# Performance work log

Hardware: AMD Instinct MI355X
Metric: run time of the kernel (lower is better)

Reference implementation:

```python
import jax, jax.numpy as jnp
import numpy as np

N = 100000   # n_nodes
D = 64       # feature dim
E = 1000000  # n_edges (avg degree 10)
L = 10       # filter_count_L
ALPHA = 0.3
EPS = 1e-8


def setup_inputs() -> dict:
    key = jax.random.key(0)
    k1, k2, k3, k4 = jax.random.split(key, 4)
    edge_src = jax.random.randint(k1, (E,), 0, N)
    edge_dst = jax.random.randint(k2, (E,), 0, N)
    # positive edge weights, scaled roughly like a degree-normalized adjacency
    edge_vals = jax.random.uniform(k3, (E,), dtype=jnp.float32) * 0.2
    X = jax.random.normal(k4, (N, D), dtype=jnp.float32)
    # hyperbolic GPR weights: alpha * (1-alpha)^(1.5*l)  (reset_parameters)
    l_idx = jnp.arange(L + 1, dtype=jnp.float32)
    manifold_weights = ALPHA * (1.0 - ALPHA) ** (l_idx * 1.5)
    return {
        "X": X,
        "edge_vals": edge_vals,
        "manifold_weights": manifold_weights,
        "edge_src": edge_src,
        "edge_dst": edge_dst,
    }


def reference(X, edge_vals, manifold_weights, edge_src, edge_dst):
    n = X.shape[0]

    def spmm(H):
        # A_tilde_n @ H with A given as COO edge list:
        # out[dst] += val * H[src]
        return jax.ops.segment_sum(edge_vals[:, None] * H[edge_src], edge_dst,
                                   num_segments=n)

    H = X
    Z = manifold_weights[0] * H  # l = 0 term
    for l in range(1, L + 1):
        H = spmm(H)
        # hyperbolic renorm: H <- H / (||H|| + eps) * tanh(||H|| + eps)
        Hn = jnp.linalg.norm(H, axis=1, keepdims=True)
        H = H / (Hn + EPS) * jnp.tanh(Hn + EPS)
        Z = Z + manifold_weights[l] * H
    return Z
```

## Files before the change

kernel.cpp:

```cpp
#include <hip/hip_runtime.h>
#include <hip/hip_fp16.h>

#define DFEAT 64
#define EPSV 1e-8f
#define CHUNK 4096
#define CAP   6144

typedef unsigned int uint;
typedef unsigned char uchar;

__device__ __forceinline__ uint h2_as_uint(__half2 h) {
    union { __half2 h; uint u; } c; c.h = h; return c.u;
}
__device__ __forceinline__ __half2 uint_as_h2(uint u) {
    union { uint u; __half2 h; } c; c.u = u; return c.h;
}
__device__ __forceinline__ uint hpack2(float lo, float hi) {
    __half2 h;
    h.x = __float2half_rn(lo);
    h.y = __float2half_rn(hi);
    return h2_as_uint(h);
}

__global__ __launch_bounds__(256) void prep_kernel(const float* __restrict__ X,
                                                   const float* __restrict__ mw,
                                                   float* __restrict__ Z,
                                                   uint* __restrict__ Xh, int nq) {
    int i = blockIdx.x * blockDim.x + threadIdx.x;
    if (i >= nq) return;
    float w0 = mw[0];
    float4 x = ((const float4*)X)[i];
    ((float4*)Z)[i] = make_float4(w0 * x.x, w0 * x.y, w0 * x.z, w0 * x.w);
    ((uint2*)Xh)[i] = make_uint2(hpack2(x.x, x.y), hpack2(x.z, x.w));
}

__global__ __launch_bounds__(256) void partial_sum_kernel(const int* __restrict__ in,
                                                          int* __restrict__ part, int n) {
    __shared__ int s[256];
    int t = threadIdx.x;
    int i = blockIdx.x * 256 + t;
    s[t] = (i < n) ? in[i] : 0;
    __syncthreads();
    for (int off = 128; off; off >>= 1) {
        if (t < off) s[t] += s[t + off];
        __syncthreads();
    }
    if (t == 0) part[blockIdx.x] = s[0];
}

__global__ __launch_bounds__(1024) void scan_partials_kernel(int* __restrict__ part, int nb) {
    __shared__ int s[1024];
    int t = threadIdx.x;
    s[t] = (t < nb) ? part[t] : 0;
    __syncthreads();
    for (int off = 1; off < 1024; off <<= 1) {
        int x = (t >= off) ? s[t - off] : 0;
        __syncthreads();
        s[t] += x;
        __syncthreads();
    }
    if (t < nb) part[t] = (t == 0) ? 0 : s[t - 1];
    if (t == 0) part[nb] = s[1023];
}

__global__ __launch_bounds__(256) void scan_final_kernel(const int* __restrict__ in,
                                                         const int* __restrict__ part,
                                                         int* __restrict__ out,
                                                         int n, int nb) {
    __shared__ int s[256];
    int b = blockIdx.x, t = threadIdx.x;
    int i = b * 256 + t;
    s[t] = (i < n) ? in[i] : 0;
    __syncthreads();
    for (int off = 1; off < 256; off <<= 1) {
        int x = (t >= off) ? s[t - off] : 0;
        __syncthreads();
        s[t] += x;
        __syncthreads();
    }
    if (i < n) out[i] = part[b] + ((t == 0) ? 0 : s[t - 1]);
    if (i == 0) out[n] = part[nb];
}

__global__ __launch_bounds__(256) void bucket_hist_kernel(const int* __restrict__ dst,
                                                          int* __restrict__ counts,
                                                          int e, int nbuck, int nblk) {
    __shared__ int h[512];
    int t = threadIdx.x, blk = blockIdx.x;
    for (int i = t; i < 512; i += 256) h[i] = 0;
    __syncthreads();
    int base = blk * CHUNK;
    #pragma unroll
    for (int k = 0; k < CHUNK / 256; ++k) {
        int i = base + k * 256 + t;
        if (i < e) atomicAdd(&h[dst[i] >> 8], 1);
    }
    __syncthreads();
    for (int b = t; b < nbuck; b += 256) counts[b * nblk + blk] = h[b];
}

__global__ __launch_bounds__(256) void bucket_scatter_kernel(
        const int* __restrict__ src, const int* __restrict__ dst,
        const float* __restrict__ val, const int* __restrict__ cbase,
        uint* __restrict__ rec, uchar* __restrict__ lrow,
        int e, int nbuck, int nblk) {
    __shared__ int cur[512];
    int t = threadIdx.x, blk = blockIdx.x;
    for (int b = t; b < nbuck; b += 256) cur[b] = cbase[b * nblk + blk];
    __syncthreads();
    int base = blk * CHUNK;
    #pragma unroll
    for (int k = 0; k < CHUNK / 256; ++k) {
        int i = base + k * 256 + t;
        if (i < e) {
            int d = dst[i];
            int b = d >> 8;
            int p = atomicAdd(&cur[b], 1);
            uint vb = (uint)__half_as_ushort(__float2half_rn(val[i])) & 0x7fffu;
            rec[p]  = (uint)src[i] | (vb << 17);
            lrow[p] = (uchar)(d & 255);
        }
    }
}

__global__ __launch_bounds__(256) void bucket_sort_kernel(
        const uint* __restrict__ rec, const uchar* __restrict__ lrow,
        const int* __restrict__ cbase, int* __restrict__ deg,
        uint* __restrict__ csr, int n, int e, int nbuck, int nblk) {
    __shared__ uint  lr[CAP];
    __shared__ uchar ll[CAP];
    __shared__ uint  so[CAP];
    __shared__ int   sc[256];
    __shared__ int   cur[256];
    int b = blockIdx.x, t = threadIdx.x;
    int s0 = cbase[b * nblk];
    int s1 = (b == nbuck - 1) ? e : cbase[(b + 1) * nblk];
    int cnt = s1 - s0;
    if (cnt > CAP) cnt = CAP;
    for (int i = t; i < cnt; i += 256) { lr[i] = rec[s0 + i]; ll[i] = lrow[s0 + i]; }
    sc[t] = 0;
    __syncthreads();
    for (int i = t; i < cnt; i += 256) atomicAdd(&sc[ll[i]], 1);
    __syncthreads();
    int row = b * 256 + t;
    int myDeg = sc[t];
    if (row < n) deg[row] = myDeg;
    for (int off = 1; off < 256; off <<= 1) {
        int x = (t >= off) ? sc[t - off] : 0;
        __syncthreads();
        sc[t] += x;
        __syncthreads();
    }
    cur[t] = sc[t] - myDeg;
    __syncthreads();
    for (int i = t; i < cnt; i += 256) {
        int p = atomicAdd(&cur[ll[i]], 1);
        so[p] = lr[i];
    }
    __syncthreads();
    for (int i = t; i < cnt; i += 256) csr[s0 + i] = so[i];
}

__global__ __launch_bounds__(256) void spmm_renorm_kernel(
        const uint* __restrict__ Hin, uint* __restrict__ Hout,
        float* __restrict__ Z, const int* __restrict__ row_ptr,
        const uint* __restrict__ csr, const float* __restrict__ mw, int l, int n) {
    int wave = (blockIdx.x * blockDim.x + threadIdx.x) >> 6;
    int lane = threadIdx.x & 63;
    int rs = lane >> 5;
    int g  = (lane >> 3) & 3;
    int lg = lane & 7;
    int row = wave * 2 + rs;
    if (wave * 2 >= n) return;
    bool valid = (row < n);
    int beg = 0, end = 0;
    if (valid) { beg = row_ptr[row]; end = row_ptr[row + 1]; }
    const uint4* H4 = (const uint4*)Hin;
    __half2 hz = uint_as_h2(0u);
    __half2 hacc[4] = {hz, hz, hz, hz};
    int j = beg + g;
    for (; j + 4 < end; j += 8) {
        uint ua = csr[j];
        uint ub = csr[j + 4];
        uint4 qa = H4[(ua & 0x1ffffu) * 8u + (uint)lg];
        uint4 qb = H4[(ub & 0x1ffffu) * 8u + (uint)lg];
        uint va = ua >> 17;
        uint vb = ub >> 17;
        __half2 va2 = uint_as_h2(va | (va << 16));
        __half2 vb2 = uint_as_h2(vb | (vb << 16));
        hacc[0] = __hfma2(va2, uint_as_h2(qa.x), hacc[0]);
        hacc[1] = __hfma2(va2, uint_as_h2(qa.y), hacc[1]);
        hacc[2] = __hfma2(va2, uint_as_h2(qa.z), hacc[2]);
        hacc[3] = __hfma2(va2, uint_as_h2(qa.w), hacc[3]);
        hacc[0] = __hfma2(vb2, uint_as_h2(qb.x), hacc[0]);
        hacc[1] = __hfma2(vb2, uint_as_h2(qb.y), hacc[1]);
        hacc[2] = __hfma2(vb2, uint_as_h2(qb.z), hacc[2]);
        hacc[3] = __hfma2(vb2, uint_as_h2(qb.w), hacc[3]);
    }
    if (j < end) {
        uint u  = csr[j];
        uint4 q = H4[(u & 0x1ffffu) * 8u + (uint)lg];
        uint v = u >> 17;
        __half2 v2 = uint_as_h2(v | (v << 16));
        hacc[0] = __hfma2(v2, uint_as_h2(q.x), hacc[0]);
        hacc[1] = __hfma2(v2, uint_as_h2(q.y), hacc[1]);
        hacc[2] = __hfma2(v2, uint_as_h2(q.z), hacc[2]);
        hacc[3] = __hfma2(v2, uint_as_h2(q.w), hacc[3]);
    }
    #pragma unroll
    for (int off = 8; off <= 16; off <<= 1) {
        #pragma unroll
        for (int k = 0; k < 4; ++k) {
            uint o = __shfl_xor(h2_as_uint(hacc[k]), off);
            hacc[k] = __hadd2(hacc[k], uint_as_h2(o));
        }
    }
    float acc[8];
    #pragma unroll
    for (int k = 0; k < 4; ++k) {
        float2 f = __half22float2(hacc[k]);
        acc[2 * k]     = f.x;
        acc[2 * k + 1] = f.y;
    }
    float sq = 0.f;
    #pragma unroll
    for (int k = 0; k < 8; ++k) sq += acc[k] * acc[k];
    #pragma unroll
    for (int off = 1; off <= 4; off <<= 1) sq += __shfl_xor(sq, off);
    float nrm = sqrtf(sq) + EPSV;
    float ex = __expf(2.0f * nrm);
    float th = 1.0f - 2.0f * __builtin_amdgcn_rcpf(ex + 1.0f);
    float scale = th * __builtin_amdgcn_rcpf(nrm);
    if (valid) {
        if (g == 0) {
            __half sh = __float2half_rn(scale);
            __half2 s2; s2.x = sh; s2.y = sh;
            uint4 o;
            o.x = h2_as_uint(__hmul2(hacc[0], s2));
            o.y = h2_as_uint(__hmul2(hacc[1], s2));
            o.z = h2_as_uint(__hmul2(hacc[2], s2));
            o.w = h2_as_uint(__hmul2(hacc[3], s2));
            ((uint4*)Hout)[(uint)row * 8u + (uint)lg] = o;
        } else if (g == 1) {
            float ws = mw[l] * scale;
            float4* Z4 = (float4*)Z;
            uint zi = (uint)row * 16u + (uint)lg * 2u;
            float4 z0 = Z4[zi];
            z0.x += ws * acc[0]; z0.y += ws * acc[1];
            z0.z += ws * acc[2]; z0.w += ws * acc[3];
            Z4[zi] = z0;
        } else if (g == 2) {
            float ws = mw[l] * scale;
            float4* Z4 = (float4*)Z;
            uint zi = (uint)row * 16u + (uint)lg * 2u + 1u;
            float4 z1 = Z4[zi];
            z1.x += ws * acc[4]; z1.y += ws * acc[5];
            z1.z += ws * acc[6]; z1.w += ws * acc[7];
            Z4[zi] = z1;
        }
    }
}

extern "C" void kernel_launch(void* const* d_in, const int* in_sizes, int n_in,
                              void* d_out, int out_size, void* d_ws, size_t ws_size,
                              hipStream_t stream) {
    const float* X         = (const float*)d_in[0];
    const float* edge_vals = (const float*)d_in[1];
    const float* mw        = (const float*)d_in[2];
    const int*   edge_src  = (const int*)d_in[3];
    const int*   edge_dst  = (const int*)d_in[4];

    int nd = in_sizes[0];
    int n  = nd / DFEAT;
    int e  = in_sizes[1];
    int L  = in_sizes[2] - 1;
    float* Z = (float*)d_out;

    int nbuck = (n + 255) >> 8;
    int nblk  = (e + CHUNK - 1) / CHUNK;
    int n1    = nbuck * nblk;

    char* ws = (char*)d_ws;
    size_t off = 0;
    auto alloc = [&](size_t bytes) -> void* {
        void* p = ws + off;
        off = (off + bytes + 255) & ~(size_t)255;
        return p;
    };
    uint*  Xh      = (uint*) alloc((size_t)nd * 2);
    uint*  Ha      = (uint*) alloc((size_t)nd * 2);
    uint*  Hb      = (uint*) alloc((size_t)nd * 2);
    uint*  csr     = (uint*) alloc((size_t)e * 4);
    uint*  rec     = (uint*) alloc((size_t)e * 4);
    uchar* lrowb   = (uchar*)alloc((size_t)e);
    int*   counts  = (int*)  alloc((size_t)(n1 + 1) * 4);
    int*   cbase   = (int*)  alloc((size_t)(n1 + 1) * 4);
    int*   deg     = (int*)  alloc((size_t)n * 4);
    int*   row_ptr = (int*)  alloc((size_t)(n + 1) * 4);
    int*   part    = (int*)  alloc((size_t)1025 * 4);

    bucket_hist_kernel<<<nblk, 256, 0, stream>>>(edge_dst, counts, e, nbuck, nblk);
    int nb1 = (n1 + 255) / 256;
    partial_sum_kernel<<<nb1, 256, 0, stream>>>(counts, part, n1);
    scan_partials_kernel<<<1, 1024, 0, stream>>>(part, nb1);
    scan_final_kernel<<<nb1, 256, 0, stream>>>(counts, part, cbase, n1, nb1);
    bucket_scatter_kernel<<<nblk, 256, 0, stream>>>(edge_src, edge_dst, edge_vals,
                                                    cbase, rec, lrowb, e, nbuck, nblk);
    bucket_sort_kernel<<<nbuck, 256, 0, stream>>>(rec, lrowb, cbase, deg, csr,
                                                  n, e, nbuck, nblk);
    int nb2 = (n + 255) / 256;
    partial_sum_kernel<<<nb2, 256, 0, stream>>>(deg, part, n);
    scan_partials_kernel<<<1, 1024, 0, stream>>>(part, nb2);
    scan_final_kernel<<<nb2, 256, 0, stream>>>(deg, part, row_ptr, n, nb2);

    int nq = nd / 4;
    prep_kernel<<<(nq + 255) / 256, 256, 0, stream>>>(X, mw, Z, Xh, nq);

    int spmm_blocks = (n + 7) / 8;
    const uint* Hin = Xh;
    uint* Hout = Ha;
    for (int l = 1; l <= L; ++l) {
        spmm_renorm_kernel<<<spmm_blocks, 256, 0, stream>>>(
            Hin, Hout, Z, row_ptr, csr, mw, l, n);
        Hin  = Hout;
        Hout = (Hout == Ha) ? Hb : Ha;
    }
}
```

Before: 444.9 us.

## Defer Z accumulation to a final combine pass over stored fp16 layers

Each propagation step now writes its renormalised fp16 H into its own slice of a new buffer instead of overwriting a ping-pong pair. The SpMM kernel no longer does an fp32 read-modify-write of Z every iteration. A single combine kernel at the end reads X and all L stored layers and writes Z once. This removes repeated full-size fp32 Z traffic per layer, at the cost of L times more workspace and a Z sum built from fp16-rounded H instead of fp32 accumulators.

```diff
diff --git a/kernel.cpp b/kernel.cpp
--- a/kernel.cpp
+++ b/kernel.cpp
@@ -23,15 +23,32 @@
 }
 
 __global__ __launch_bounds__(256) void prep_kernel(const float* __restrict__ X,
-                                                   const float* __restrict__ mw,
-                                                   float* __restrict__ Z,
                                                    uint* __restrict__ Xh, int nq) {
+    int i = blockIdx.x * blockDim.x + threadIdx.x;
+    if (i >= nq) return;
+    float4 x = ((const float4*)X)[i];
+    ((uint2*)Xh)[i] = make_uint2(hpack2(x.x, x.y), hpack2(x.z, x.w));
+}
+
+__global__ __launch_bounds__(256) void combine_kernel(
+        const float* __restrict__ X, const uint* __restrict__ Hall,
+        const float* __restrict__ mw, float* __restrict__ Z,
+        int nq, int sliceu2, int L) {
     int i = blockIdx.x * blockDim.x + threadIdx.x;
     if (i >= nq) return;
     float w0 = mw[0];
     float4 x = ((const float4*)X)[i];
-    ((float4*)Z)[i] = make_float4(w0 * x.x, w0 * x.y, w0 * x.z, w0 * x.w);
-    ((uint2*)Xh)[i] = make_uint2(hpack2(x.x, x.y), hpack2(x.z, x.w));
+    float4 z = make_float4(w0 * x.x, w0 * x.y, w0 * x.z, w0 * x.w);
+    const uint2* H2 = (const uint2*)Hall;
+    for (int l = 1; l <= L; ++l) {
+        float wl = mw[l];
+        uint2 h = H2[(size_t)(l - 1) * sliceu2 + i];
+        float2 a = __half22float2(uint_as_h2(h.x));
+        float2 b = __half22float2(uint_as_h2(h.y));
+        z.x += wl * a.x; z.y += wl * a.y;
+        z.z += wl * b.x; z.w += wl * b.y;
+    }
+    ((float4*)Z)[i] = z;
 }
 
 __global__ __launch_bounds__(256) void partial_sum_kernel(const int* __restrict__ in,
@@ -163,8 +180,7 @@
 
 __global__ __launch_bounds__(256) void spmm_renorm_kernel(
         const uint* __restrict__ Hin, uint* __restrict__ Hout,
-        float* __restrict__ Z, const int* __restrict__ row_ptr,
-        const uint* __restrict__ csr, const float* __restrict__ mw, int l, int n) {
+        const int* __restrict__ row_ptr, const uint* __restrict__ csr, int n) {
     int wave = (blockIdx.x * blockDim.x + threadIdx.x) >> 6;
     int lane = threadIdx.x & 63;
     int rs = lane >> 5;
@@ -215,49 +231,27 @@
             hacc[k] = __hadd2(hacc[k], uint_as_h2(o));
         }
     }
-    float acc[8];
+    float sq = 0.f;
     #pragma unroll
     for (int k = 0; k < 4; ++k) {
         float2 f = __half22float2(hacc[k]);
-        acc[2 * k]     = f.x;
-        acc[2 * k + 1] = f.y;
-    }
-    float sq = 0.f;
-    #pragma unroll
-    for (int k = 0; k < 8; ++k) sq += acc[k] * acc[k];
+        sq += f.x * f.x + f.y * f.y;
+    }
     #pragma unroll
     for (int off = 1; off <= 4; off <<= 1) sq += __shfl_xor(sq, off);
     float nrm = sqrtf(sq) + EPSV;
     float ex = __expf(2.0f * nrm);
     float th = 1.0f - 2.0f * __builtin_amdgcn_rcpf(ex + 1.0f);
     float scale = th * __builtin_amdgcn_rcpf(nrm);
-    if (valid) {
-        if (g == 0) {
-            __half sh = __float2half_rn(scale);
-            __half2 s2; s2.x = sh; s2.y = sh;
-            uint4 o;
-            o.x = h2_as_uint(__hmul2(hacc[0], s2));
-            o.y = h2_as_uint(__hmul2(hacc[1], s2));
-            o.z = h2_as_uint(__hmul2(hacc[2], s2));
-            o.w = h2_as_uint(__hmul2(hacc[3], s2));
-            ((uint4*)Hout)[(uint)row * 8u + (uint)lg] = o;
-        } else if (g == 1) {
-            float ws = mw[l] * scale;
-            float4* Z4 = (float4*)Z;
-            uint zi = (uint)row * 16u + (uint)lg * 2u;
-            float4 z0 = Z4[zi];
-            z0.x += ws * acc[0]; z0.y += ws * acc[1];
-            z0.z += ws * acc[2]; z0.w += ws * acc[3];
-            Z4[zi] = z0;
-        } else if (g == 2) {
-            float ws = mw[l] * scale;
-            float4* Z4 = (float4*)Z;
-            uint zi = (uint)row * 16u + (uint)lg * 2u + 1u;
-            float4 z1 = Z4[zi];
-            z1.x += ws * acc[4]; z1.y += ws * acc[5];
-            z1.z += ws * acc[6]; z1.w += ws * acc[7];
-            Z4[zi] = z1;
-        }
+    if (valid && g == 0) {
+        __half sh = __float2half_rn(scale);
+        __half2 s2; s2.x = sh; s2.y = sh;
+        uint4 o;
+        o.x = h2_as_uint(__hmul2(hacc[0], s2));
+        o.y = h2_as_uint(__hmul2(hacc[1], s2));
+        o.z = h2_as_uint(__hmul2(hacc[2], s2));
+        o.w = h2_as_uint(__hmul2(hacc[3], s2));
+        ((uint4*)Hout)[(uint)row * 8u + (uint)lg] = o;
     }
 }
 
@@ -288,8 +282,7 @@
         return p;
     };
     uint*  Xh      = (uint*) alloc((size_t)nd * 2);
-    uint*  Ha      = (uint*) alloc((size_t)nd * 2);
-    uint*  Hb      = (uint*) alloc((size_t)nd * 2);
+    uint*  Hall    = (uint*) alloc((size_t)nd * 2 * L);
     uint*  csr     = (uint*) alloc((size_t)e * 4);
     uint*  rec     = (uint*) alloc((size_t)e * 4);
     uchar* lrowb   = (uchar*)alloc((size_t)e);
@@ -314,15 +307,18 @@
     scan_final_kernel<<<nb2, 256, 0, stream>>>(deg, part, row_ptr, n, nb2);
 
     int nq = nd / 4;
-    prep_kernel<<<(nq + 255) / 256, 256, 0, stream>>>(X, mw, Z, Xh, nq);
+    prep_kernel<<<(nq + 255) / 256, 256, 0, stream>>>(X, Xh, nq);
 
     int spmm_blocks = (n + 7) / 8;
+    int sliceu = nd / 2;
     const uint* Hin = Xh;
-    uint* Hout = Ha;
     for (int l = 1; l <= L; ++l) {
+        uint* Hout = Hall + (size_t)(l - 1) * sliceu;
         spmm_renorm_kernel<<<spmm_blocks, 256, 0, stream>>>(
-            Hin, Hout, Z, row_ptr, csr, mw, l, n);
-        Hin  = Hout;
-        Hout = (Hout == Ha) ? Hb : Ha;
-    }
-}
+            Hin, Hout, row_ptr, csr, n);
+        Hin = Hout;
+    }
+
+    combine_kernel<<<(nq + 255) / 256, 256, 0, stream>>>(
+        X, Hall, mw, Z, nq, sliceu / 2, L);
+}
```

New measurement: 411.3 us. -7.6%, faster.
